# Optimization experiments

Hardware: AMD Instinct MI355X
Metric: run time of the kernel (lower is better)

Reference implementation:

```python
import jax, jax.numpy as jnp
import numpy as np

N, K, D = 262144, 256, 128
SCALE = 0.1
LOG2PI = float(np.log(2.0 * np.pi))


def setup_inputs() -> dict:
    key = jax.random.key(0)
    k_in, k_mu, k_ls, k_noise = jax.random.split(key, 4)
    return {
        "input": jax.random.normal(k_in, (N, D), dtype=jnp.float32),
        "means": jax.random.normal(k_mu, (K, D), dtype=jnp.float32),
        "log_stds": jax.random.normal(k_ls, (K, D), dtype=jnp.float32) * 0.5,
        "weights": jnp.ones((K,), dtype=jnp.float32),
        "noise": jax.random.normal(k_noise, (N, D), dtype=jnp.float32),
    }


def _gmm_forward(x, means, log_stds, weights, noise):
    d = x.shape[-1]
    # Diagonal-Gaussian log-prob per component, via GEMM decomposition:
    inv_var = jnp.exp(-2.0 * log_stds)                      # [K, D]
    quad = (
        (x * x) @ inv_var.T                                  # [N, K]
        - 2.0 * (x @ (means * inv_var).T)                    # [N, K]
        + jnp.sum(means * means * inv_var, axis=-1)          # [K]
    )
    log_p_x_z = -0.5 * (quad + d * LOG2PI) - jnp.sum(log_stds, axis=-1)  # [N, K]
    log_p_z = jax.nn.log_softmax(weights)                    # [K]
    joint = log_p_x_z + log_p_z                              # [N, K]
    p_z_x = jax.nn.softmax(joint + 1e-8, axis=-1)            # [N, K]
    idxs = jnp.argmax(p_z_x, axis=-1)                        # [N]
    Q = jnp.mean(jax.lax.stop_gradient(p_z_x) * joint)       # scalar
    # Resample from the selected component (noise replaces randn_like)
    resampled_x = means[idxs] + jnp.exp(log_stds[idxs]) * noise * SCALE
    return resampled_x, idxs, Q


def reference(input, means, log_stds, weights, noise):
    return _gmm_forward(input, means, log_stds, weights, noise)
```

## Files before the change

### kernel.cpp

```cpp
#include <hip/hip_runtime.h>
#include <math.h>

#define N_ROWS 262144
#define K_COMP 256
#define D_DIM  128
#define BN 64
#define KIN 256

typedef _Float16 half8v __attribute__((ext_vector_type(8)));
typedef _Float16 half4v __attribute__((ext_vector_type(4)));
typedef float    f32x4  __attribute__((ext_vector_type(4)));

static __device__ __constant__ float kLOG2PI = 1.8378770664093453f;

__global__ __launch_bounds__(128) void gmm_prep(
    const float* __restrict__ means, const float* __restrict__ log_stds,
    const float* __restrict__ weights,
    _Float16* __restrict__ Bhi, _Float16* __restrict__ Blo,
    float* __restrict__ sigma, float* __restrict__ ck, double* __restrict__ wsq)
{
    int k = blockIdx.x;
    int d = threadIdx.x;
    float ls = log_stds[k * D_DIM + d];
    float mu = means[k * D_DIM + d];
    float iv = expf(-2.0f * ls);
    float m2 = -2.0f * mu * iv;
    sigma[k * D_DIM + d] = expf(ls);

    {
        int c = k >> 4;
        #pragma unroll
        for (int t = 0; t < 2; ++t) {
            int kin = t * 128 + d;
            float val = t ? m2 : iv;
            int s = kin >> 5;
            int l = ((kin >> 3) & 3) * 16 + (k & 15);
            int j = kin & 7;
            int lin = ((c * 8 + s) * 64 + l) * 8 + j;
            _Float16 hi = (_Float16)val;
            Bhi[lin] = hi;
            Blo[lin] = (_Float16)(val - (float)hi);
        }
    }

    float c = mu * mu * iv;
    float s = ls;
    float w1 = weights[d], w2 = weights[d + 128];
    float wm = fmaxf(w1, w2);

    __shared__ float red[8];
    int lane = d & 63, wv = d >> 6;
    #pragma unroll
    for (int o = 32; o > 0; o >>= 1) {
        c += __shfl_down(c, o, 64);
        s += __shfl_down(s, o, 64);
        wm = fmaxf(wm, __shfl_down(wm, o, 64));
    }
    if (lane == 0) { red[wv] = c; red[2 + wv] = s; red[4 + wv] = wm; }
    __syncthreads();
    float csum = red[0] + red[1];
    float ssum = red[2] + red[3];
    float wmax = fmaxf(red[4], red[5]);
    float we = expf(w1 - wmax) + expf(w2 - wmax);
    #pragma unroll
    for (int o = 32; o > 0; o >>= 1) we += __shfl_down(we, o, 64);
    if (lane == 0) red[6 + wv] = we;
    __syncthreads();
    if (d == 0) {
        float wsum = red[6] + red[7];
        float lw = weights[k] - (wmax + logf(wsum));
        ck[k] = -0.5f * (csum + (float)D_DIM * kLOG2PI) - ssum + lw;
        if (k == 0) *wsq = 0.0;
    }
}

__global__ __launch_bounds__(256, 2) void gmm_main(
    const float* __restrict__ x, const float* __restrict__ noise,
    const float* __restrict__ means, const float* __restrict__ sigma,
    const _Float16* __restrict__ Bhi, const _Float16* __restrict__ Blo,
    const float* __restrict__ ck,
    float* __restrict__ out_x, float* __restrict__ out_idx, double* __restrict__ wsq)
{
    __shared__ char  sA[2][BN * 512];
    __shared__ float sCk[K_COMP];
    __shared__ float sMax[BN][4];
    __shared__ int   sAm [BN][4];
    __shared__ float sEs [BN][4];
    __shared__ float sQs [BN][4];
    __shared__ int   sIdx[BN];

    const int tid = threadIdx.x;
    const int w   = tid >> 6;
    const int l   = tid & 63;
    const int lm  = l & 15;
    const int lh  = l >> 4;
    const long n0 = (long)blockIdx.x * BN;

    sCk[tid] = ck[tid];

    {
        const float4* xg = (const float4*)(x + (size_t)n0 * D_DIM);
        #pragma unroll
        for (int it = 0; it < 8; ++it) {
            int g = it * 256 + tid;
            int row = g >> 5, d4 = g & 31;
            float4 xv = xg[g];
            float xe[4] = {xv.x, xv.y, xv.z, xv.w};
            half4v x2h, x2l, xh, xl;
            #pragma unroll
            for (int cc = 0; cc < 4; ++cc) {
                float v = xe[cc], vv = v * v;
                _Float16 a = (_Float16)vv;
                x2h[cc] = a; x2l[cc] = (_Float16)(vv - (float)a);
                _Float16 b = (_Float16)v;
                xh[cc] = b;  xl[cc] = (_Float16)(v - (float)b);
            }
            unsigned sw = (unsigned)(row & 7) << 4;
            unsigned o0 = ((unsigned)(row * 512 + d4 * 8)) ^ sw;
            unsigned o1 = ((unsigned)(row * 512 + 256 + d4 * 8)) ^ sw;
            *(half4v*)(sA[0] + o0) = x2h;
            *(half4v*)(sA[0] + o1) = xh;
            *(half4v*)(sA[1] + o0) = x2l;
            *(half4v*)(sA[1] + o1) = xl;
        }
    }
    __syncthreads();

    f32x4 acc[4][4];
    #pragma unroll
    for (int rf = 0; rf < 4; ++rf)
        #pragma unroll
        for (int cf = 0; cf < 4; ++cf)
            acc[rf][cf] = (f32x4){0.0f, 0.0f, 0.0f, 0.0f};

    const half8v* Bh = (const half8v*)Bhi;
    const half8v* Bl = (const half8v*)Blo;

    #pragma unroll 2
    for (int s = 0; s < 8; ++s) {
        half8v ah[4], al[4], bh[4], bl[4];
        #pragma unroll
        for (int rf = 0; rf < 4; ++rf) {
            int row = rf * 16 + lm;
            unsigned off = ((unsigned)(row * 512 + s * 64 + lh * 16))
                         ^ ((unsigned)(row & 7) << 4);
            ah[rf] = *(const half8v*)(sA[0] + off);
            al[rf] = *(const half8v*)(sA[1] + off);
        }
        #pragma unroll
        for (int cf = 0; cf < 4; ++cf) {
            int cgl = w * 4 + cf;
            int bidx = (cgl * 8 + s) * 64 + l;
            bh[cf] = Bh[bidx];
            bl[cf] = Bl[bidx];
        }
        #pragma unroll
        for (int rf = 0; rf < 4; ++rf)
            #pragma unroll
            for (int cf = 0; cf < 4; ++cf) {
                acc[rf][cf] = __builtin_amdgcn_mfma_f32_16x16x32_f16(ah[rf], bh[cf], acc[rf][cf], 0, 0, 0);
                acc[rf][cf] = __builtin_amdgcn_mfma_f32_16x16x32_f16(ah[rf], bl[cf], acc[rf][cf], 0, 0, 0);
                acc[rf][cf] = __builtin_amdgcn_mfma_f32_16x16x32_f16(al[rf], bh[cf], acc[rf][cf], 0, 0, 0);
            }
    }

    float ckv[4];
    #pragma unroll
    for (int cf = 0; cf < 4; ++cf) ckv[cf] = sCk[w * 64 + cf * 16 + lm];

    #pragma unroll
    for (int rf = 0; rf < 4; ++rf) {
        #pragma unroll
        for (int reg = 0; reg < 4; ++reg) {
            int row = rf * 16 + lh * 4 + reg;
            float jv[4];
            float m = -INFINITY; int am = 0;
            #pragma unroll
            for (int cf = 0; cf < 4; ++cf) {
                float v = fmaf(-0.5f, acc[rf][cf][reg], ckv[cf]);
                jv[cf] = v;
                int col = w * 64 + cf * 16 + lm;
                if (v > m) { m = v; am = col; }
            }
            #pragma unroll
            for (int o = 1; o < 16; o <<= 1) {
                float om = __shfl_xor(m, o, 16);
                int   oa = __shfl_xor(am, o, 16);
                if (om > m || (om == m && oa < am)) { m = om; am = oa; }
            }
            float es = 0.0f, qs = 0.0f;
            #pragma unroll
            for (int cf = 0; cf < 4; ++cf) {
                float e = expf(jv[cf] - m);
                es += e; qs = fmaf(e, jv[cf], qs);
            }
            #pragma unroll
            for (int o = 1; o < 16; o <<= 1) {
                es += __shfl_xor(es, o, 16);
                qs += __shfl_xor(qs, o, 16);
            }
            if (lm == 0) {
                sMax[row][w] = m; sAm[row][w] = am;
                sEs [row][w] = es; sQs[row][w] = qs;
            }
        }
    }
    __syncthreads();

    if (tid < BN) {
        const int row = tid;
        float m = sMax[row][0]; int am = sAm[row][0];
        float es = sEs[row][0], qs = sQs[row][0];
        #pragma unroll
        for (int w2 = 1; w2 < 4; ++w2) {
            float mw = sMax[row][w2];
            if (mw > m) {
                float f = expf(m - mw);
                es = es * f + sEs[row][w2];
                qs = qs * f + sQs[row][w2];
                m = mw; am = sAm[row][w2];
            } else {
                float f = expf(mw - m);
                es += sEs[row][w2] * f;
                qs += sQs[row][w2] * f;
            }
        }
        sIdx[row] = am;
        float q = qs / es;
        #pragma unroll
        for (int o = 1; o < 64; o <<= 1) q += __shfl_xor(q, o, 64);
        if (tid == 0) atomicAdd(wsq, (double)q);
    }
    __syncthreads();

    const int wv = tid >> 6, lane = tid & 63;
    #pragma unroll 4
    for (int r16 = 0; r16 < 16; ++r16) {
        const int row = wv * 16 + r16;
        const int idx = sIdx[row];
        const long n = n0 + row;
        float2 mv = *(const float2*)&means[idx * D_DIM + lane * 2];
        float2 sv = *(const float2*)&sigma[idx * D_DIM + lane * 2];
        float2 nv = *(const float2*)&noise[n * D_DIM + lane * 2];
        float2 ov;
        ov.x = mv.x + sv.x * nv.x * 0.1f;
        ov.y = mv.y + sv.y * nv.y * 0.1f;
        *(float2*)&out_x[n * D_DIM + lane * 2] = ov;
    }
    if (tid < BN) out_idx[n0 + tid] = (float)sIdx[tid];
}

__global__ void gmm_finalize(const double* __restrict__ wsq, float* __restrict__ out_q)
{
    *out_q = (float)(*wsq * (1.0 / ((double)N_ROWS * (double)K_COMP)));
}

extern "C" void kernel_launch(void* const* d_in, const int* in_sizes, int n_in,
                              void* d_out, int out_size, void* d_ws, size_t ws_size,
                              hipStream_t stream)
{
    const float* x        = (const float*)d_in[0];
    const float* means    = (const float*)d_in[1];
    const float* log_stds = (const float*)d_in[2];
    const float* weights  = (const float*)d_in[3];
    const float* noise    = (const float*)d_in[4];

    float* out_x   = (float*)d_out;
    float* out_idx = (float*)d_out + (size_t)N_ROWS * D_DIM;
    float* out_q   = out_idx + N_ROWS;

    float*     ws    = (float*)d_ws;
    _Float16*  Bhi   = (_Float16*)ws;
    _Float16*  Blo   = (_Float16*)(ws + 32768);
    float*     sigma = ws + 65536;
    float*     ckp   = ws + 98304;
    double*    wsq   = (double*)(ws + 98560);

    hipLaunchKernelGGL(gmm_prep, dim3(K_COMP), dim3(D_DIM), 0, stream,
                       means, log_stds, weights, Bhi, Blo, sigma, ckp, wsq);
    hipLaunchKernelGGL(gmm_main, dim3(N_ROWS / BN), dim3(256), 0, stream,
                       x, noise, means, sigma, Bhi, Blo, ckp, out_x, out_idx, wsq);
    hipLaunchKernelGGL(gmm_finalize, dim3(1), dim3(1), 0, stream, wsq, out_q);
}
```

Measured before the change: 461.2 us.

## Halve A-tile LDS by staging x^2 then x in two passes, raise occupancy

```diff
diff --git a/kernel.cpp b/kernel.cpp
--- a/kernel.cpp
+++ b/kernel.cpp
@@ -74,14 +74,14 @@
     }
 }
 
-__global__ __launch_bounds__(256, 2) void gmm_main(
+__global__ __launch_bounds__(256, 3) void gmm_main(
     const float* __restrict__ x, const float* __restrict__ noise,
     const float* __restrict__ means, const float* __restrict__ sigma,
     const _Float16* __restrict__ Bhi, const _Float16* __restrict__ Blo,
     const float* __restrict__ ck,
     float* __restrict__ out_x, float* __restrict__ out_idx, double* __restrict__ wsq)
 {
-    __shared__ char  sA[2][BN * 512];
+    __shared__ char  sA[2][BN * 256];
     __shared__ float sCk[K_COMP];
     __shared__ float sMax[BN][4];
     __shared__ int   sAm [BN][4];
@@ -98,31 +98,28 @@
 
     sCk[tid] = ck[tid];
 
+    float4 xv[8];
     {
         const float4* xg = (const float4*)(x + (size_t)n0 * D_DIM);
         #pragma unroll
-        for (int it = 0; it < 8; ++it) {
-            int g = it * 256 + tid;
-            int row = g >> 5, d4 = g & 31;
-            float4 xv = xg[g];
-            float xe[4] = {xv.x, xv.y, xv.z, xv.w};
-            half4v x2h, x2l, xh, xl;
-            #pragma unroll
-            for (int cc = 0; cc < 4; ++cc) {
-                float v = xe[cc], vv = v * v;
-                _Float16 a = (_Float16)vv;
-                x2h[cc] = a; x2l[cc] = (_Float16)(vv - (float)a);
-                _Float16 b = (_Float16)v;
-                xh[cc] = b;  xl[cc] = (_Float16)(v - (float)b);
-            }
-            unsigned sw = (unsigned)(row & 7) << 4;
-            unsigned o0 = ((unsigned)(row * 512 + d4 * 8)) ^ sw;
-            unsigned o1 = ((unsigned)(row * 512 + 256 + d4 * 8)) ^ sw;
-            *(half4v*)(sA[0] + o0) = x2h;
-            *(half4v*)(sA[0] + o1) = xh;
-            *(half4v*)(sA[1] + o0) = x2l;
-            *(half4v*)(sA[1] + o1) = xl;
-        }
+        for (int it = 0; it < 8; ++it) xv[it] = xg[it * 256 + tid];
+    }
+
+    #pragma unroll
+    for (int it = 0; it < 8; ++it) {
+        int g = it * 256 + tid;
+        int row = g >> 5, d4 = g & 31;
+        float xe[4] = {xv[it].x, xv[it].y, xv[it].z, xv[it].w};
+        half4v h, lo;
+        #pragma unroll
+        for (int cc = 0; cc < 4; ++cc) {
+            float vv = xe[cc] * xe[cc];
+            _Float16 a = (_Float16)vv;
+            h[cc] = a; lo[cc] = (_Float16)(vv - (float)a);
+        }
+        unsigned off = ((unsigned)(row * 256 + d4 * 8)) ^ ((unsigned)(row & 7) << 4);
+        *(half4v*)(sA[0] + off) = h;
+        *(half4v*)(sA[1] + off) = lo;
     }
     __syncthreads();
 
@@ -137,30 +134,75 @@
     const half8v* Bl = (const half8v*)Blo;
 
     #pragma unroll 2
-    for (int s = 0; s < 8; ++s) {
-        half8v ah[4], al[4], bh[4], bl[4];
+    for (int s = 0; s < 4; ++s) {
+        half8v ah[4], al[4], bh4[4], bl4[4];
         #pragma unroll
         for (int rf = 0; rf < 4; ++rf) {
             int row = rf * 16 + lm;
-            unsigned off = ((unsigned)(row * 512 + s * 64 + lh * 16))
+            unsigned off = ((unsigned)(row * 256 + s * 64 + lh * 16))
                          ^ ((unsigned)(row & 7) << 4);
             ah[rf] = *(const half8v*)(sA[0] + off);
             al[rf] = *(const half8v*)(sA[1] + off);
         }
         #pragma unroll
         for (int cf = 0; cf < 4; ++cf) {
-            int cgl = w * 4 + cf;
-            int bidx = (cgl * 8 + s) * 64 + l;
-            bh[cf] = Bh[bidx];
-            bl[cf] = Bl[bidx];
+            int bidx = ((w * 4 + cf) * 8 + s) * 64 + l;
+            bh4[cf] = Bh[bidx];
+            bl4[cf] = Bl[bidx];
         }
         #pragma unroll
         for (int rf = 0; rf < 4; ++rf)
             #pragma unroll
             for (int cf = 0; cf < 4; ++cf) {
-                acc[rf][cf] = __builtin_amdgcn_mfma_f32_16x16x32_f16(ah[rf], bh[cf], acc[rf][cf], 0, 0, 0);
-                acc[rf][cf] = __builtin_amdgcn_mfma_f32_16x16x32_f16(ah[rf], bl[cf], acc[rf][cf], 0, 0, 0);
-                acc[rf][cf] = __builtin_amdgcn_mfma_f32_16x16x32_f16(al[rf], bh[cf], acc[rf][cf], 0, 0, 0);
+                acc[rf][cf] = __builtin_amdgcn_mfma_f32_16x16x32_f16(ah[rf], bh4[cf], acc[rf][cf], 0, 0, 0);
+                acc[rf][cf] = __builtin_amdgcn_mfma_f32_16x16x32_f16(ah[rf], bl4[cf], acc[rf][cf], 0, 0, 0);
+                acc[rf][cf] = __builtin_amdgcn_mfma_f32_16x16x32_f16(al[rf], bh4[cf], acc[rf][cf], 0, 0, 0);
+            }
+    }
+    __syncthreads();
+
+    #pragma unroll
+    for (int it = 0; it < 8; ++it) {
+        int g = it * 256 + tid;
+        int row = g >> 5, d4 = g & 31;
+        float xe[4] = {xv[it].x, xv[it].y, xv[it].z, xv[it].w};
+        half4v h, lo;
+        #pragma unroll
+        for (int cc = 0; cc < 4; ++cc) {
+            float v = xe[cc];
+            _Float16 a = (_Float16)v;
+            h[cc] = a; lo[cc] = (_Float16)(v - (float)a);
+        }
+        unsigned off = ((unsigned)(row * 256 + d4 * 8)) ^ ((unsigned)(row & 7) << 4);
+        *(half4v*)(sA[0] + off) = h;
+        *(half4v*)(sA[1] + off) = lo;
+    }
+    __syncthreads();
+
+    #pragma unroll 2
+    for (int s = 4; s < 8; ++s) {
+        half8v ah[4], al[4], bh4[4], bl4[4];
+        #pragma unroll
+        for (int rf = 0; rf < 4; ++rf) {
+            int row = rf * 16 + lm;
+            unsigned off = ((unsigned)(row * 256 + (s - 4) * 64 + lh * 16))
+                         ^ ((unsigned)(row & 7) << 4);
+            ah[rf] = *(const half8v*)(sA[0] + off);
+            al[rf] = *(const half8v*)(sA[1] + off);
+        }
+        #pragma unroll
+        for (int cf = 0; cf < 4; ++cf) {
+            int bidx = ((w * 4 + cf) * 8 + s) * 64 + l;
+            bh4[cf] = Bh[bidx];
+            bl4[cf] = Bl[bidx];
+        }
+        #pragma unroll
+        for (int rf = 0; rf < 4; ++rf)
+            #pragma unroll
+            for (int cf = 0; cf < 4; ++cf) {
+                acc[rf][cf] = __builtin_amdgcn_mfma_f32_16x16x32_f16(ah[rf], bh4[cf], acc[rf][cf], 0, 0, 0);
+                acc[rf][cf] = __builtin_amdgcn_mfma_f32_16x16x32_f16(ah[rf], bl4[cf], acc[rf][cf], 0, 0, 0);
+                acc[rf][cf] = __builtin_amdgcn_mfma_f32_16x16x32_f16(al[rf], bh4[cf], acc[rf][cf], 0, 0, 0);
             }
     }
 
```

Result: no change. 469.4 us (+1.8%).

## Double-buffer A staging across K halves, prefetch noise, raise occupancy

Applied to the files above, without the earlier changes.

```diff
diff --git a/kernel.cpp b/kernel.cpp
--- a/kernel.cpp
+++ b/kernel.cpp
@@ -74,14 +74,15 @@
     }
 }
 
-__global__ __launch_bounds__(256, 2) void gmm_main(
+__global__ __launch_bounds__(256, 3) void gmm_main(
     const float* __restrict__ x, const float* __restrict__ noise,
     const float* __restrict__ means, const float* __restrict__ sigma,
     const _Float16* __restrict__ Bhi, const _Float16* __restrict__ Blo,
     const float* __restrict__ ck,
     float* __restrict__ out_x, float* __restrict__ out_idx, double* __restrict__ wsq)
 {
-    __shared__ char  sA[2][BN * 512];
+    __shared__ char  sAhi[2][BN * 128];
+    __shared__ char  sAlo[2][BN * 128];
     __shared__ float sCk[K_COMP];
     __shared__ float sMax[BN][4];
     __shared__ int   sAm [BN][4];
@@ -98,33 +99,53 @@
 
     sCk[tid] = ck[tid];
 
-    {
-        const float4* xg = (const float4*)(x + (size_t)n0 * D_DIM);
-        #pragma unroll
-        for (int it = 0; it < 8; ++it) {
-            int g = it * 256 + tid;
-            int row = g >> 5, d4 = g & 31;
-            float4 xv = xg[g];
-            float xe[4] = {xv.x, xv.y, xv.z, xv.w};
-            half4v x2h, x2l, xh, xl;
-            #pragma unroll
-            for (int cc = 0; cc < 4; ++cc) {
-                float v = xe[cc], vv = v * v;
-                _Float16 a = (_Float16)vv;
-                x2h[cc] = a; x2l[cc] = (_Float16)(vv - (float)a);
-                _Float16 b = (_Float16)v;
-                xh[cc] = b;  xl[cc] = (_Float16)(v - (float)b);
-            }
-            unsigned sw = (unsigned)(row & 7) << 4;
-            unsigned o0 = ((unsigned)(row * 512 + d4 * 8)) ^ sw;
-            unsigned o1 = ((unsigned)(row * 512 + 256 + d4 * 8)) ^ sw;
-            *(half4v*)(sA[0] + o0) = x2h;
-            *(half4v*)(sA[0] + o1) = xh;
-            *(half4v*)(sA[1] + o0) = x2l;
-            *(half4v*)(sA[1] + o1) = xl;
-        }
-    }
-    __syncthreads();
+    const float* xb = x + (size_t)n0 * D_DIM;
+    float4 pv[4];
+
+#define LOADP(D0) { \
+    _Pragma("unroll") \
+    for (int it = 0; it < 4; ++it) { \
+        int g = it * 256 + tid; int r = g >> 4, c4 = g & 15; \
+        pv[it] = *(const float4*)&xb[r * D_DIM + (D0) + c4 * 4]; } }
+
+#define STAGE(B, SQ) { \
+    _Pragma("unroll") \
+    for (int it = 0; it < 4; ++it) { \
+        int g = it * 256 + tid; int r = g >> 4, c4 = g & 15; \
+        float xe[4] = {pv[it].x, pv[it].y, pv[it].z, pv[it].w}; \
+        half4v h, lo; \
+        _Pragma("unroll") \
+        for (int cc = 0; cc < 4; ++cc) { \
+            float v = (SQ) ? xe[cc] * xe[cc] : xe[cc]; \
+            _Float16 a = (_Float16)v; \
+            h[cc] = a; lo[cc] = (_Float16)(v - (float)a); } \
+        unsigned off = ((unsigned)(r * 128 + c4 * 8)) ^ ((unsigned)(r & 7) << 4); \
+        *(half4v*)(sAhi[B] + off) = h; \
+        *(half4v*)(sAlo[B] + off) = lo; } }
+
+#define COMPUTE(B, SBASE) { \
+    _Pragma("unroll") \
+    for (int ss = 0; ss < 2; ++ss) { \
+        int s = (SBASE) + ss; \
+        half8v ah[4], al[4], bh4[4], bl4[4]; \
+        _Pragma("unroll") \
+        for (int rf = 0; rf < 4; ++rf) { \
+            int row = rf * 16 + lm; \
+            unsigned off = ((unsigned)(row * 128 + ss * 64 + lh * 16)) \
+                         ^ ((unsigned)(row & 7) << 4); \
+            ah[rf] = *(const half8v*)(sAhi[B] + off); \
+            al[rf] = *(const half8v*)(sAlo[B] + off); } \
+        _Pragma("unroll") \
+        for (int cf = 0; cf < 4; ++cf) { \
+            int bidx = ((w * 4 + cf) * 8 + s) * 64 + l; \
+            bh4[cf] = Bh[bidx]; bl4[cf] = Bl[bidx]; } \
+        _Pragma("unroll") \
+        for (int rf = 0; rf < 4; ++rf) \
+            _Pragma("unroll") \
+            for (int cf = 0; cf < 4; ++cf) { \
+                acc[rf][cf] = __builtin_amdgcn_mfma_f32_16x16x32_f16(ah[rf], bh4[cf], acc[rf][cf], 0, 0, 0); \
+                acc[rf][cf] = __builtin_amdgcn_mfma_f32_16x16x32_f16(ah[rf], bl4[cf], acc[rf][cf], 0, 0, 0); \
+                acc[rf][cf] = __builtin_amdgcn_mfma_f32_16x16x32_f16(al[rf], bh4[cf], acc[rf][cf], 0, 0, 0); } } }
 
     f32x4 acc[4][4];
     #pragma unroll
@@ -136,33 +157,15 @@
     const half8v* Bh = (const half8v*)Bhi;
     const half8v* Bl = (const half8v*)Blo;
 
-    #pragma unroll 2
-    for (int s = 0; s < 8; ++s) {
-        half8v ah[4], al[4], bh[4], bl[4];
-        #pragma unroll
-        for (int rf = 0; rf < 4; ++rf) {
-            int row = rf * 16 + lm;
-            unsigned off = ((unsigned)(row * 512 + s * 64 + lh * 16))
-                         ^ ((unsigned)(row & 7) << 4);
-            ah[rf] = *(const half8v*)(sA[0] + off);
-            al[rf] = *(const half8v*)(sA[1] + off);
-        }
-        #pragma unroll
-        for (int cf = 0; cf < 4; ++cf) {
-            int cgl = w * 4 + cf;
-            int bidx = (cgl * 8 + s) * 64 + l;
-            bh[cf] = Bh[bidx];
-            bl[cf] = Bl[bidx];
-        }
-        #pragma unroll
-        for (int rf = 0; rf < 4; ++rf)
-            #pragma unroll
-            for (int cf = 0; cf < 4; ++cf) {
-                acc[rf][cf] = __builtin_amdgcn_mfma_f32_16x16x32_f16(ah[rf], bh[cf], acc[rf][cf], 0, 0, 0);
-                acc[rf][cf] = __builtin_amdgcn_mfma_f32_16x16x32_f16(ah[rf], bl[cf], acc[rf][cf], 0, 0, 0);
-                acc[rf][cf] = __builtin_amdgcn_mfma_f32_16x16x32_f16(al[rf], bh[cf], acc[rf][cf], 0, 0, 0);
-            }
-    }
+    LOADP(0)  STAGE(0, 1)
+    __syncthreads();
+    LOADP(64) COMPUTE(0, 0) STAGE(1, 1)
+    __syncthreads();
+    LOADP(0)  COMPUTE(1, 2) STAGE(0, 0)
+    __syncthreads();
+    LOADP(64) COMPUTE(0, 4) STAGE(1, 0)
+    __syncthreads();
+    COMPUTE(1, 6)
 
     float ckv[4];
     #pragma unroll
@@ -191,7 +194,7 @@
             float es = 0.0f, qs = 0.0f;
             #pragma unroll
             for (int cf = 0; cf < 4; ++cf) {
-                float e = expf(jv[cf] - m);
+                float e = __expf(jv[cf] - m);
                 es += e; qs = fmaf(e, jv[cf], qs);
             }
             #pragma unroll
@@ -205,8 +208,16 @@
             }
         }
     }
-    __syncthreads();
-
+
+    const int wv = tid >> 6, lane = tid & 63;
+    float2 nvv[16];
+    #pragma unroll
+    for (int r16 = 0; r16 < 16; ++r16)
+        nvv[r16] = *(const float2*)&noise[(n0 + wv * 16 + r16) * D_DIM + lane * 2];
+
+    __syncthreads();
+
+    float qv = 0.0f;
     if (tid < BN) {
         const int row = tid;
         float m = sMax[row][0]; int am = sAm[row][0];
@@ -215,39 +226,39 @@
         for (int w2 = 1; w2 < 4; ++w2) {
             float mw = sMax[row][w2];
             if (mw > m) {
-                float f = expf(m - mw);
+                float f = __expf(m - mw);
                 es = es * f + sEs[row][w2];
                 qs = qs * f + sQs[row][w2];
                 m = mw; am = sAm[row][w2];
             } else {
-                float f = expf(mw - m);
+                float f = __expf(mw - m);
                 es += sEs[row][w2] * f;
                 qs += sQs[row][w2] * f;
             }
         }
         sIdx[row] = am;
-        float q = qs / es;
+        float q = __fdividef(qs, es);
         #pragma unroll
         for (int o = 1; o < 64; o <<= 1) q += __shfl_xor(q, o, 64);
-        if (tid == 0) atomicAdd(wsq, (double)q);
-    }
-    __syncthreads();
-
-    const int wv = tid >> 6, lane = tid & 63;
-    #pragma unroll 4
+        qv = q;
+    }
+    __syncthreads();
+
+    #pragma unroll
     for (int r16 = 0; r16 < 16; ++r16) {
         const int row = wv * 16 + r16;
         const int idx = sIdx[row];
         const long n = n0 + row;
         float2 mv = *(const float2*)&means[idx * D_DIM + lane * 2];
         float2 sv = *(const float2*)&sigma[idx * D_DIM + lane * 2];
-        float2 nv = *(const float2*)&noise[n * D_DIM + lane * 2];
         float2 ov;
-        ov.x = mv.x + sv.x * nv.x * 0.1f;
-        ov.y = mv.y + sv.y * nv.y * 0.1f;
+        ov.x = mv.x + sv.x * nvv[r16].x * 0.1f;
+        ov.y = mv.y + sv.y * nvv[r16].y * 0.1f;
         *(float2*)&out_x[n * D_DIM + lane * 2] = ov;
     }
     if (tid < BN) out_idx[n0 + tid] = (float)sIdx[tid];
+
+    if (tid == 0) atomicAdd(wsq, (double)qv);
 }
 
 __global__ void gmm_finalize(const double* __restrict__ wsq, float* __restrict__ out_q)
```

Result: faster. 441.9 us (-4.2%).

## Give each wave its own 32 rows over all components, removing LDS staging

Applied to the files above, without the earlier changes.

```diff
diff --git a/kernel.cpp b/kernel.cpp
--- a/kernel.cpp
+++ b/kernel.cpp
@@ -4,11 +4,10 @@
 #define N_ROWS 262144
 #define K_COMP 256
 #define D_DIM  128
-#define BN 64
+#define WROWS 32
 #define KIN 256
 
 typedef _Float16 half8v __attribute__((ext_vector_type(8)));
-typedef _Float16 half4v __attribute__((ext_vector_type(4)));
 typedef float    f32x4  __attribute__((ext_vector_type(4)));
 
 static __device__ __constant__ float kLOG2PI = 1.8378770664093453f;
@@ -81,105 +80,80 @@
     const float* __restrict__ ck,
     float* __restrict__ out_x, float* __restrict__ out_idx, double* __restrict__ wsq)
 {
-    __shared__ char  sA[2][BN * 512];
-    __shared__ float sCk[K_COMP];
-    __shared__ float sMax[BN][4];
-    __shared__ int   sAm [BN][4];
-    __shared__ float sEs [BN][4];
-    __shared__ float sQs [BN][4];
-    __shared__ int   sIdx[BN];
-
     const int tid = threadIdx.x;
-    const int w   = tid >> 6;
+    const int wv  = tid >> 6;
     const int l   = tid & 63;
     const int lm  = l & 15;
     const int lh  = l >> 4;
-    const long n0 = (long)blockIdx.x * BN;
-
-    sCk[tid] = ck[tid];
-
-    {
-        const float4* xg = (const float4*)(x + (size_t)n0 * D_DIM);
-        #pragma unroll
-        for (int it = 0; it < 8; ++it) {
-            int g = it * 256 + tid;
-            int row = g >> 5, d4 = g & 31;
-            float4 xv = xg[g];
-            float xe[4] = {xv.x, xv.y, xv.z, xv.w};
-            half4v x2h, x2l, xh, xl;
-            #pragma unroll
-            for (int cc = 0; cc < 4; ++cc) {
-                float v = xe[cc], vv = v * v;
-                _Float16 a = (_Float16)vv;
-                x2h[cc] = a; x2l[cc] = (_Float16)(vv - (float)a);
-                _Float16 b = (_Float16)v;
-                xh[cc] = b;  xl[cc] = (_Float16)(v - (float)b);
-            }
-            unsigned sw = (unsigned)(row & 7) << 4;
-            unsigned o0 = ((unsigned)(row * 512 + d4 * 8)) ^ sw;
-            unsigned o1 = ((unsigned)(row * 512 + 256 + d4 * 8)) ^ sw;
-            *(half4v*)(sA[0] + o0) = x2h;
-            *(half4v*)(sA[0] + o1) = xh;
-            *(half4v*)(sA[1] + o0) = x2l;
-            *(half4v*)(sA[1] + o1) = xl;
-        }
-    }
-    __syncthreads();
-
-    f32x4 acc[4][4];
-    #pragma unroll
-    for (int rf = 0; rf < 4; ++rf)
-        #pragma unroll
-        for (int cf = 0; cf < 4; ++cf)
-            acc[rf][cf] = (f32x4){0.0f, 0.0f, 0.0f, 0.0f};
-
+    const long n0 = ((long)blockIdx.x * 4 + wv) * WROWS;
+
+    const float* xw = x + (size_t)n0 * D_DIM;
     const half8v* Bh = (const half8v*)Bhi;
     const half8v* Bl = (const half8v*)Blo;
 
-    #pragma unroll 2
-    for (int s = 0; s < 8; ++s) {
-        half8v ah[4], al[4], bh[4], bl[4];
+    f32x4 acc[2][16];
+    #pragma unroll
+    for (int rf = 0; rf < 2; ++rf)
         #pragma unroll
-        for (int rf = 0; rf < 4; ++rf) {
-            int row = rf * 16 + lm;
-            unsigned off = ((unsigned)(row * 512 + s * 64 + lh * 16))
-                         ^ ((unsigned)(row & 7) << 4);
-            ah[rf] = *(const half8v*)(sA[0] + off);
-            al[rf] = *(const half8v*)(sA[1] + off);
-        }
-        #pragma unroll
-        for (int cf = 0; cf < 4; ++cf) {
-            int cgl = w * 4 + cf;
-            int bidx = (cgl * 8 + s) * 64 + l;
-            bh[cf] = Bh[bidx];
-            bl[cf] = Bl[bidx];
-        }
-        #pragma unroll
-        for (int rf = 0; rf < 4; ++rf)
-            #pragma unroll
-            for (int cf = 0; cf < 4; ++cf) {
-                acc[rf][cf] = __builtin_amdgcn_mfma_f32_16x16x32_f16(ah[rf], bh[cf], acc[rf][cf], 0, 0, 0);
-                acc[rf][cf] = __builtin_amdgcn_mfma_f32_16x16x32_f16(ah[rf], bl[cf], acc[rf][cf], 0, 0, 0);
-                acc[rf][cf] = __builtin_amdgcn_mfma_f32_16x16x32_f16(al[rf], bh[cf], acc[rf][cf], 0, 0, 0);
-            }
-    }
-
-    float ckv[4];
-    #pragma unroll
-    for (int cf = 0; cf < 4; ++cf) ckv[cf] = sCk[w * 64 + cf * 16 + lm];
-
-    #pragma unroll
-    for (int rf = 0; rf < 4; ++rf) {
+        for (int cf = 0; cf < 16; ++cf)
+            acc[rf][cf] = (f32x4){0.0f, 0.0f, 0.0f, 0.0f};
+
+#define ALOAD(dst0, dst1, rf, d0) \
+    dst0 = *(const float4*)&xw[((rf) * 16 + lm) * D_DIM + (d0) + lh * 8]; \
+    dst1 = *(const float4*)&xw[((rf) * 16 + lm) * D_DIM + (d0) + lh * 8 + 4];
+
+#define ACVT(ah_, al_, a0, a1, SQ) { \
+    float xe[8] = {a0.x, a0.y, a0.z, a0.w, a1.x, a1.y, a1.z, a1.w}; \
+    _Pragma("unroll") \
+    for (int j = 0; j < 8; ++j) { \
+        float v = (SQ) ? xe[j] * xe[j] : xe[j]; \
+        _Float16 h = (_Float16)v; \
+        ah_[j] = h; al_[j] = (_Float16)(v - (float)h); } }
+
+#define KHALF(SQ, SBIAS) { \
+    float4 c00, c01, c10, c11, p00, p01, p10, p11; \
+    ALOAD(c00, c01, 0, 0) ALOAD(c10, c11, 1, 0) \
+    _Pragma("unroll 1") \
+    for (int ss = 0; ss < 4; ++ss) { \
+        if (ss < 3) { ALOAD(p00, p01, 0, (ss + 1) * 32) ALOAD(p10, p11, 1, (ss + 1) * 32) } \
+        half8v ah[2], al[2]; \
+        ACVT(ah[0], al[0], c00, c01, SQ) \
+        ACVT(ah[1], al[1], c10, c11, SQ) \
+        int s = ss + (SBIAS); \
+        _Pragma("unroll") \
+        for (int cf = 0; cf < 16; ++cf) { \
+            int bidx = (cf * 8 + s) * 64 + l; \
+            half8v bh = Bh[bidx], bl = Bl[bidx]; \
+            _Pragma("unroll") \
+            for (int rf = 0; rf < 2; ++rf) { \
+                acc[rf][cf] = __builtin_amdgcn_mfma_f32_16x16x32_f16(ah[rf], bh, acc[rf][cf], 0, 0, 0); \
+                acc[rf][cf] = __builtin_amdgcn_mfma_f32_16x16x32_f16(ah[rf], bl, acc[rf][cf], 0, 0, 0); \
+                acc[rf][cf] = __builtin_amdgcn_mfma_f32_16x16x32_f16(al[rf], bh, acc[rf][cf], 0, 0, 0); \
+            } \
+        } \
+        c00 = p00; c01 = p01; c10 = p10; c11 = p11; \
+    } }
+
+    KHALF(1, 0)
+    KHALF(0, 4)
+
+    float ckv[16];
+    #pragma unroll
+    for (int cf = 0; cf < 16; ++cf) ckv[cf] = ck[cf * 16 + lm];
+
+    int amreg[2][4];
+    float qacc = 0.0f;
+    #pragma unroll
+    for (int rf = 0; rf < 2; ++rf) {
         #pragma unroll
         for (int reg = 0; reg < 4; ++reg) {
-            int row = rf * 16 + lh * 4 + reg;
-            float jv[4];
+            float jv[16];
             float m = -INFINITY; int am = 0;
             #pragma unroll
-            for (int cf = 0; cf < 4; ++cf) {
+            for (int cf = 0; cf < 16; ++cf) {
                 float v = fmaf(-0.5f, acc[rf][cf][reg], ckv[cf]);
                 jv[cf] = v;
-                int col = w * 64 + cf * 16 + lm;
+                int col = cf * 16 + lm;
                 if (v > m) { m = v; am = col; }
             }
             #pragma unroll
@@ -190,8 +164,8 @@
             }
             float es = 0.0f, qs = 0.0f;
             #pragma unroll
-            for (int cf = 0; cf < 4; ++cf) {
-                float e = expf(jv[cf] - m);
+            for (int cf = 0; cf < 16; ++cf) {
+                float e = __expf(jv[cf] - m);
                 es += e; qs = fmaf(e, jv[cf], qs);
             }
             #pragma unroll
@@ -199,55 +173,34 @@
                 es += __shfl_xor(es, o, 16);
                 qs += __shfl_xor(qs, o, 16);
             }
-            if (lm == 0) {
-                sMax[row][w] = m; sAm[row][w] = am;
-                sEs [row][w] = es; sQs[row][w] = qs;
-            }
+            if (lm == 0) qacc += __fdividef(qs, es);
+            amreg[rf][reg] = am;
         }
     }
-    __syncthreads();
-
-    if (tid < BN) {
-        const int row = tid;
-        float m = sMax[row][0]; int am = sAm[row][0];
-        float es = sEs[row][0], qs = sQs[row][0];
-        #pragma unroll
-        for (int w2 = 1; w2 < 4; ++w2) {
-            float mw = sMax[row][w2];
-            if (mw > m) {
-                float f = expf(m - mw);
-                es = es * f + sEs[row][w2];
-                qs = qs * f + sQs[row][w2];
-                m = mw; am = sAm[row][w2];
-            } else {
-                float f = expf(mw - m);
-                es += sEs[row][w2] * f;
-                qs += sQs[row][w2] * f;
-            }
-        }
-        sIdx[row] = am;
-        float q = qs / es;
-        #pragma unroll
-        for (int o = 1; o < 64; o <<= 1) q += __shfl_xor(q, o, 64);
-        if (tid == 0) atomicAdd(wsq, (double)q);
-    }
-    __syncthreads();
-
-    const int wv = tid >> 6, lane = tid & 63;
-    #pragma unroll 4
-    for (int r16 = 0; r16 < 16; ++r16) {
-        const int row = wv * 16 + r16;
-        const int idx = sIdx[row];
-        const long n = n0 + row;
-        float2 mv = *(const float2*)&means[idx * D_DIM + lane * 2];
-        float2 sv = *(const float2*)&sigma[idx * D_DIM + lane * 2];
-        float2 nv = *(const float2*)&noise[n * D_DIM + lane * 2];
+    #pragma unroll
+    for (int o = 1; o < 64; o <<= 1) qacc += __shfl_xor(qacc, o, 64);
+
+    int idxmine = 0;
+    #pragma unroll
+    for (int r = 0; r < WROWS; ++r) {
+        const int rf = r >> 4, lhr = (r >> 2) & 3, reg = r & 3;
+        const int idx = __shfl(amreg[rf][reg], lhr * 16, 64);
+        if (l == r) idxmine = idx;
+        const long n = n0 + r;
+        float2 mv = *(const float2*)&means[idx * D_DIM + l * 2];
+        float2 sv = *(const float2*)&sigma[idx * D_DIM + l * 2];
+        float2 nv = *(const float2*)&noise[n * D_DIM + l * 2];
         float2 ov;
         ov.x = mv.x + sv.x * nv.x * 0.1f;
         ov.y = mv.y + sv.y * nv.y * 0.1f;
-        *(float2*)&out_x[n * D_DIM + lane * 2] = ov;
-    }
-    if (tid < BN) out_idx[n0 + tid] = (float)sIdx[tid];
+        *(float2*)&out_x[n * D_DIM + l * 2] = ov;
+    }
+    if (l < WROWS) out_idx[n0 + l] = (float)idxmine;
+    if (l == 0) atomicAdd(wsq, (double)qacc);
+
+#undef ALOAD
+#undef ACVT
+#undef KHALF
 }
 
 __global__ void gmm_finalize(const double* __restrict__ wsq, float* __restrict__ out_q)
@@ -278,7 +231,7 @@
 
     hipLaunchKernelGGL(gmm_prep, dim3(K_COMP), dim3(D_DIM), 0, stream,
                        means, log_stds, weights, Bhi, Blo, sigma, ckp, wsq);
-    hipLaunchKernelGGL(gmm_main, dim3(N_ROWS / BN), dim3(256), 0, stream,
+    hipLaunchKernelGGL(gmm_main, dim3(N_ROWS / (WROWS * 4)), dim3(256), 0, stream,
                        x, noise, means, sigma, Bhi, Blo, ckp, out_x, out_idx, wsq);
     hipLaunchKernelGGL(gmm_finalize, dim3(1), dim3(1), 0, stream, wsq, out_q);
 }
```

Measured after the change: 488.3 us. 1.06x slower.
